# Kernel tuning notes

Measured on AMD Instinct MI355X. Metric: run time of the kernel, lower is better.

The kernel has to match this reference:

```python
import jax, jax.numpy as jnp
import numpy as np

B, S, D = 8, 1024, 1024   # batch, routed-over rows, feature dim (input_dim)
E = 1024                  # output_dim (== S so gather indices are in range)
K = 2                     # top-k
ALPHA = 0.01


def setup_inputs() -> dict:
    key = jax.random.key(0)
    kx, kw = jax.random.split(key)
    x = jax.random.normal(kx, (B, S, D), dtype=jnp.float32)
    # nn.Linear(input_dim, output_dim, bias=False) weight: [E, D]
    W = jax.random.normal(kw, (E, D), dtype=jnp.float32) / np.sqrt(D).astype(np.float32)
    return {"x": x, "W": W}


def reference(x, W):
    # logits = proj(x): [B, S, E]  (temperature == 1.0 -> no scaling)
    logits = jnp.einsum('bsd,ed->bse', x, W)
    probs = jax.nn.softmax(logits, axis=-1)
    topk_probs, topk_idx = jax.lax.top_k(probs, K)            # [B, S, K]
    # router_selections: gather rows of x along dim 1 -> [B, S, K, D]
    sel = x[jnp.arange(B)[:, None, None], topk_idx]
    # y = sum_k topk_probs * selected rows -> [B, S, D]
    y = jnp.einsum('bsk,bskd->bsd', topk_probs, sel)
    # auxiliary load-balance loss
    router_probs = probs.mean(axis=(0, 1))                    # [E]
    counts = jnp.bincount(topk_idx.reshape(-1), length=E).astype(probs.dtype)
    router_fraction = counts / counts.sum()
    aux_loss = ALPHA * E * jnp.sum(router_probs * router_fraction)
    return y, aux_loss
```

## Files before the change

### kernel.cpp

```cpp
#include <hip/hip_runtime.h>

#define MTOK 8192
#define ED   1024

typedef short s16x8 __attribute__((ext_vector_type(8)));
typedef float f32x4 __attribute__((ext_vector_type(4)));
typedef int   i32x4 __attribute__((ext_vector_type(4)));
typedef unsigned short u16x4 __attribute__((ext_vector_type(4)));

__device__ __forceinline__ unsigned short f2bf(float f) {
    unsigned u = __builtin_bit_cast(unsigned, f);
    u += 0x7fff + ((u >> 16) & 1);
    return (unsigned short)(u >> 16);
}
__device__ __forceinline__ float bf2f(unsigned short h) {
    unsigned u = ((unsigned)h) << 16;
    return __builtin_bit_cast(float, u);
}

__global__ __launch_bounds__(256) void split_bf16_kernel(
        const float* __restrict__ src, unsigned short* __restrict__ hi,
        unsigned short* __restrict__ lo, int n4) {
    int idx = blockIdx.x * 256 + threadIdx.x;
    const int stride = gridDim.x * 256;
    for (; idx < n4; idx += stride) {
        float4 v = ((const float4*)src)[idx];
        u16x4 h, l;
        h[0] = f2bf(v.x); l[0] = f2bf(v.x - bf2f(h[0]));
        h[1] = f2bf(v.y); l[1] = f2bf(v.y - bf2f(h[1]));
        h[2] = f2bf(v.z); l[2] = f2bf(v.z - bf2f(h[2]));
        h[3] = f2bf(v.w); l[3] = f2bf(v.w - bf2f(h[3]));
        ((u16x4*)hi)[idx] = h;
        ((u16x4*)lo)[idx] = l;
    }
}

__device__ __forceinline__ void gload16(const void* g, void* l) {
    __builtin_amdgcn_global_load_lds(
        (const __attribute__((address_space(1))) void*)g,
        (__attribute__((address_space(3))) void*)l, 16, 0, 0);
}

__device__ __forceinline__ int cvtpk(float a, float b) {
    int r;
    asm("v_cvt_pk_bf16_f32 %0, %1, %2" : "=v"(r) : "v"(a), "v"(b));
    return r;
}

__global__ __launch_bounds__(256, 2) void gemm_mfma_split_kernel(
        const float* __restrict__ Xf,
        const unsigned short* __restrict__ Whi, const unsigned short* __restrict__ Wlo,
        float* __restrict__ C) {
    __shared__ __align__(16) unsigned char smem[2 * 32768];

    const int bid = blockIdx.x;
    const int xcd = bid & 7;
    const int j   = bid >> 3;
    const int bm  = xcd * 8 + (j >> 3);
    const int bn  = j & 7;

    const int tid  = threadIdx.x;
    const int lane = tid & 63;
    const int wid  = tid >> 6;

    const float* gsrcF = Xf + (size_t)(bm * 128 + wid * 64 + (lane & 15)) * ED
                            + (lane >> 4) * 8;
    const int srow = lane >> 2;
    const int sg   = (lane & 3) ^ ((srow >> 1) & 3);
    const unsigned short* gsrcS =
        ((wid == 3) ? Wlo : Whi) + (size_t)(bn * 128 + srow) * ED + sg * 8;
    unsigned char* const dstU = smem + ((wid < 2) ? wid * 8192
                                                  : 16384 + (wid - 2) * 8192);

#define STAGE(buf, kk)                                                          \
    if (wid < 2) {                                                              \
        _Pragma("unroll")                                                       \
        for (int c = 0; c < 8; ++c)                                             \
            gload16(gsrcF + (kk) + (c >> 1) * (16 * ED) + (c & 1) * 4,          \
                    dstU + (buf) * 32768 + c * 1024);                           \
    } else {                                                                    \
        _Pragma("unroll")                                                       \
        for (int c = 0; c < 8; ++c)                                             \
            gload16(gsrcS + (kk) + c * (16 * ED),                               \
                    dstU + (buf) * 32768 + c * 1024);                           \
    }

    const int wm = wid >> 1, wn = wid & 1;
    const int fr = lane & 15, fg = lane >> 4;
    const int pg = fg ^ ((fr >> 1) & 3);
    const int boff  = ((wn * 64 + fr) * 32 + pg * 8) * 2;
    const int aoffb = wm * 8192 + lane * 16;

    f32x4 acc[4][4] = {};

    STAGE(0, 0);
    asm volatile("s_waitcnt vmcnt(0)" ::: "memory");
    __builtin_amdgcn_s_barrier();

    for (int t = 0; t < 32; ++t) {
        const int cur = t & 1;
        if (t < 31) STAGE(cur ^ 1, (t + 1) * 32);

        const unsigned char* bufb = smem + cur * 32768;

        s16x8 ah[4], al[4], bh[4], bl[4];
#pragma unroll
        for (int i = 0; i < 4; ++i) {
            const float4 f0 = *(const float4*)(bufb + aoffb + i * 2048);
            const float4 f1 = *(const float4*)(bufb + aoffb + i * 2048 + 1024);
            i32x4 h, l;
            h[0] = cvtpk(f0.x, f0.y);
            h[1] = cvtpk(f0.z, f0.w);
            h[2] = cvtpk(f1.x, f1.y);
            h[3] = cvtpk(f1.z, f1.w);
            l[0] = cvtpk(f0.x - __builtin_bit_cast(float, h[0] << 16),
                         f0.y - __builtin_bit_cast(float, h[0] & 0xffff0000));
            l[1] = cvtpk(f0.z - __builtin_bit_cast(float, h[1] << 16),
                         f0.w - __builtin_bit_cast(float, h[1] & 0xffff0000));
            l[2] = cvtpk(f1.x - __builtin_bit_cast(float, h[2] << 16),
                         f1.y - __builtin_bit_cast(float, h[2] & 0xffff0000));
            l[3] = cvtpk(f1.z - __builtin_bit_cast(float, h[3] << 16),
                         f1.w - __builtin_bit_cast(float, h[3] & 0xffff0000));
            ah[i] = __builtin_bit_cast(s16x8, h);
            al[i] = __builtin_bit_cast(s16x8, l);
            bh[i] = *(const s16x8*)(bufb + 16384 + boff + i * 1024);
            bl[i] = *(const s16x8*)(bufb + 24576 + boff + i * 1024);
        }
#pragma unroll
        for (int i = 0; i < 4; ++i)
#pragma unroll
            for (int jj = 0; jj < 4; ++jj) {
                acc[i][jj] = __builtin_amdgcn_mfma_f32_16x16x32_bf16(ah[i], bh[jj], acc[i][jj], 0, 0, 0);
                acc[i][jj] = __builtin_amdgcn_mfma_f32_16x16x32_bf16(ah[i], bl[jj], acc[i][jj], 0, 0, 0);
                acc[i][jj] = __builtin_amdgcn_mfma_f32_16x16x32_bf16(al[i], bh[jj], acc[i][jj], 0, 0, 0);
            }

        asm volatile("s_waitcnt vmcnt(0) lgkmcnt(0)" ::: "memory");
        __builtin_amdgcn_s_barrier();
    }
#undef STAGE

    const int crow = bm * 128 + wm * 64 + fg * 4;
    const int ccol = bn * 128 + wn * 64 + fr;
#pragma unroll
    for (int i = 0; i < 4; ++i)
#pragma unroll
        for (int jj = 0; jj < 4; ++jj)
#pragma unroll
            for (int r = 0; r < 4; ++r)
                C[(size_t)(crow + i * 16 + r) * ED + ccol + jj * 16] = acc[i][jj][r];
}

#define BM 128
#define BN 128
#define BK 32
#define LDA (BM + 4)
#define LDB (BN + 4)

__global__ __launch_bounds__(256) void gemm_logits_kernel(const float* __restrict__ X,
                                                          const float* __restrict__ W,
                                                          float* __restrict__ C) {
    __shared__ float As[BK][LDA];
    __shared__ float Bs[BK][LDB];
    const int bm  = blockIdx.y * BM;
    const int bn  = blockIdx.x * BN;
    const int tid = threadIdx.x;
    const int tx  = tid & 15;
    const int ty  = tid >> 4;
    const int lr  = tid >> 3;
    const int lc  = (tid & 7) << 2;

    float acc[8][8];
#pragma unroll
    for (int i = 0; i < 8; ++i)
#pragma unroll
        for (int j = 0; j < 8; ++j) acc[i][j] = 0.f;

    for (int k0 = 0; k0 < ED; k0 += BK) {
#pragma unroll
        for (int i = 0; i < 4; ++i) {
            const int r = lr + i * 32;
            float4 va = *(const float4*)&X[(size_t)(bm + r) * ED + k0 + lc];
            As[lc + 0][r] = va.x; As[lc + 1][r] = va.y;
            As[lc + 2][r] = va.z; As[lc + 3][r] = va.w;
            float4 vb = *(const float4*)&W[(size_t)(bn + r) * ED + k0 + lc];
            Bs[lc + 0][r] = vb.x; Bs[lc + 1][r] = vb.y;
            Bs[lc + 2][r] = vb.z; Bs[lc + 3][r] = vb.w;
        }
        __syncthreads();
#pragma unroll
        for (int kk = 0; kk < BK; ++kk) {
            float a[8], b[8];
            *(float4*)&a[0] = *(const float4*)&As[kk][ty * 8];
            *(float4*)&a[4] = *(const float4*)&As[kk][ty * 8 + 4];
            *(float4*)&b[0] = *(const float4*)&Bs[kk][tx * 8];
            *(float4*)&b[4] = *(const float4*)&Bs[kk][tx * 8 + 4];
#pragma unroll
            for (int i = 0; i < 8; ++i)
#pragma unroll
                for (int j = 0; j < 8; ++j)
                    acc[i][j] = fmaf(a[i], b[j], acc[i][j]);
        }
        __syncthreads();
    }
#pragma unroll
    for (int i = 0; i < 8; ++i) {
        const int r = bm + ty * 8 + i;
        float4* dst = (float4*)&C[(size_t)r * ED + bn + tx * 8];
        dst[0] = make_float4(acc[i][0], acc[i][1], acc[i][2], acc[i][3]);
        dst[1] = make_float4(acc[i][4], acc[i][5], acc[i][6], acc[i][7]);
    }
}

__device__ __forceinline__ bool better(float v, int i, float bv, int bi) {
    return (v > bv) || (v == bv && i < bi);
}

__global__ __launch_bounds__(256, 8) void softmax_wave_kernel(
        const float* __restrict__ X, float* __restrict__ OUT,
        float* __restrict__ partial, int* __restrict__ counts) {
    __shared__ float L[4 * 1024];
    const int tid  = threadIdx.x;
    const int lane = tid & 63;
    const int w    = tid >> 6;
    const int t    = blockIdx.x * 4 + w;

    const float4* row4 = (const float4*)&OUT[(size_t)t * ED];
    float4 p[4];
#pragma unroll
    for (int i = 0; i < 4; ++i) p[i] = row4[lane + 64 * i];

    float v1 = -1e30f, v2 = -1e30f; int i1 = 0x7fffffff, i2 = 0x7fffffff;
#pragma unroll
    for (int i = 0; i < 4; ++i) {
        const float vv[4] = {p[i].x, p[i].y, p[i].z, p[i].w};
#pragma unroll
        for (int c = 0; c < 4; ++c) {
            const int e = 256 * i + 4 * lane + c;
            const float v = vv[c];
            if (better(v, e, v1, i1)) { v2 = v1; i2 = i1; v1 = v; i1 = e; }
            else if (better(v, e, v2, i2)) { v2 = v; i2 = e; }
        }
    }
#pragma unroll
    for (int off = 32; off; off >>= 1) {
        const float ov1 = __shfl_xor(v1, off); const int oi1 = __shfl_xor(i1, off);
        const float ov2 = __shfl_xor(v2, off); const int oi2 = __shfl_xor(i2, off);
        if (better(ov1, oi1, v1, i1)) {
            float nv2; int ni2;
            if (better(v1, i1, ov2, oi2)) { nv2 = v1; ni2 = i1; }
            else { nv2 = ov2; ni2 = oi2; }
            v1 = ov1; i1 = oi1; v2 = nv2; i2 = ni2;
        } else if (better(ov1, oi1, v2, i2)) { v2 = ov1; i2 = oi1; }
    }
    const float m = v1;

    float s = 0.f;
#pragma unroll
    for (int i = 0; i < 4; ++i) {
        p[i].x = __expf(p[i].x - m); p[i].y = __expf(p[i].y - m);
        p[i].z = __expf(p[i].z - m); p[i].w = __expf(p[i].w - m);
        s += p[i].x + p[i].y + p[i].z + p[i].w;
    }
#pragma unroll
    for (int off = 32; off; off >>= 1) s += __shfl_xor(s, off);
    const float inv = 1.f / s;

#pragma unroll
    for (int i = 0; i < 4; ++i) {
        float4 q = make_float4(p[i].x * inv, p[i].y * inv, p[i].z * inv, p[i].w * inv);
        *(float4*)&L[w * 1024 + i * 256 + lane * 4] = q;
    }

    const float p1 = inv;
    const float p2 = __expf(v2 - m) * inv;
    const int b = t >> 10;
    const float4* x1 = (const float4*)&X[((size_t)(b << 10) + i1) * ED];
    const float4* x2 = (const float4*)&X[((size_t)(b << 10) + i2) * ED];
    float4* yrow = (float4*)&OUT[(size_t)t * ED];
#pragma unroll
    for (int i = 0; i < 4; ++i) {
        const int idx = lane + 64 * i;
        const float4 a = x1[idx];
        const float4 c = x2[idx];
        float4 r;
        r.x = fmaf(p1, a.x, p2 * c.x);
        r.y = fmaf(p1, a.y, p2 * c.y);
        r.z = fmaf(p1, a.z, p2 * c.z);
        r.w = fmaf(p1, a.w, p2 * c.w);
        yrow[idx] = r;
    }

    if (lane == 0) { atomicAdd(&counts[i1], 1); atomicAdd(&counts[i2], 1); }

    __syncthreads();
    float4 s0 = *(float4*)&L[0 * 1024 + tid * 4];
    float4 s1 = *(float4*)&L[1 * 1024 + tid * 4];
    float4 s2 = *(float4*)&L[2 * 1024 + tid * 4];
    float4 s3 = *(float4*)&L[3 * 1024 + tid * 4];
    float4 r;
    r.x = (s0.x + s1.x) + (s2.x + s3.x);
    r.y = (s0.y + s1.y) + (s2.y + s3.y);
    r.z = (s0.z + s1.z) + (s2.z + s3.z);
    r.w = (s0.w + s1.w) + (s2.w + s3.w);
    *(float4*)&partial[(size_t)blockIdx.x * 1024 + tid * 4] = r;
}

__global__ __launch_bounds__(256) void aux1_kernel(const float* __restrict__ partial,
                                                   const int* __restrict__ counts,
                                                   float* __restrict__ dotPartial) {
    __shared__ float red[16][16];
    const int tid = threadIdx.x;
    const int el  = tid & 15;
    const int ch  = tid >> 4;
    const int e   = blockIdx.x * 16 + el;
    float s = 0.f;
    for (int k = 0; k < 128; ++k)
        s += partial[(size_t)(ch * 128 + k) * 1024 + e];
    red[ch][el] = s;
    __syncthreads();
    if (tid < 16) {
        float rs = 0.f;
#pragma unroll
        for (int c = 0; c < 16; ++c) rs += red[c][tid];
        float val = rs * (float)counts[blockIdx.x * 16 + tid];
#pragma unroll
        for (int off = 8; off; off >>= 1) val += __shfl_xor(val, off);
        if (tid == 0) dotPartial[blockIdx.x] = val;
    }
}

__global__ void aux2_kernel(const float* __restrict__ dotPartial, float* __restrict__ out) {
    const int lane = threadIdx.x;
    float v = dotPartial[lane];
#pragma unroll
    for (int off = 32; off; off >>= 1) v += __shfl_xor(v, off);
    if (lane == 0)
        out[(size_t)MTOK * ED] = v * (0.01f * 1024.f / (8192.f * 16384.f));
}

#define TOKS_PER_BLK 16
__global__ __launch_bounds__(256) void softmax_topk_y_kernel(
        const float* __restrict__ X, float* __restrict__ OUT,
        float* __restrict__ router_sum, int* __restrict__ counts) {
    __shared__ float routerLocal[ED];
    __shared__ float redMax[4];
    __shared__ float redSum[4];
    __shared__ float wV1[4]; __shared__ int wI1[4];
    __shared__ float wV2[4]; __shared__ int wI2[4];

    const int tid  = threadIdx.x;
    const int lane = tid & 63;
    const int wave = tid >> 6;

    for (int e = tid; e < ED; e += 256) routerLocal[e] = 0.f;
    __syncthreads();

    const int t0 = blockIdx.x * TOKS_PER_BLK;
    for (int t = t0; t < t0 + TOKS_PER_BLK; ++t) {
        const float* lrow = &OUT[(size_t)t * ED];
        float l[4];
#pragma unroll
        for (int i = 0; i < 4; ++i) l[i] = lrow[tid + i * 256];

        float m = fmaxf(fmaxf(l[0], l[1]), fmaxf(l[2], l[3]));
#pragma unroll
        for (int off = 32; off; off >>= 1) m = fmaxf(m, __shfl_xor(m, off));
        if (lane == 0) redMax[wave] = m;
        __syncthreads();
        m = fmaxf(fmaxf(redMax[0], redMax[1]), fmaxf(redMax[2], redMax[3]));

        float p[4]; float s = 0.f;
#pragma unroll
        for (int i = 0; i < 4; ++i) { p[i] = expf(l[i] - m); s += p[i]; }
#pragma unroll
        for (int off = 32; off; off >>= 1) s += __shfl_xor(s, off);
        if (lane == 0) redSum[wave] = s;

        float v1 = -1e30f, v2 = -1e30f; int i1 = 0x7fffffff, i2 = 0x7fffffff;
#pragma unroll
        for (int i = 0; i < 4; ++i) {
            const float v = l[i]; const int ix = tid + i * 256;
            if (better(v, ix, v1, i1)) { v2 = v1; i2 = i1; v1 = v; i1 = ix; }
            else if (better(v, ix, v2, i2)) { v2 = v; i2 = ix; }
        }
#pragma unroll
        for (int off = 32; off; off >>= 1) {
            const float ov1 = __shfl_xor(v1, off); const int oi1 = __shfl_xor(i1, off);
            const float ov2 = __shfl_xor(v2, off); const int oi2 = __shfl_xor(i2, off);
            if (better(ov1, oi1, v1, i1)) {
                float nv2; int ni2;
                if (better(v1, i1, ov2, oi2)) { nv2 = v1; ni2 = i1; }
                else { nv2 = ov2; ni2 = oi2; }
                v1 = ov1; i1 = oi1; v2 = nv2; i2 = ni2;
            } else if (better(ov1, oi1, v2, i2)) { v2 = ov1; i2 = oi1; }
        }
        if (lane == 0) { wV1[wave] = v1; wI1[wave] = i1; wV2[wave] = v2; wI2[wave] = i2; }
        __syncthreads();

        v1 = wV1[0]; i1 = wI1[0]; v2 = wV2[0]; i2 = wI2[0];
#pragma unroll
        for (int w = 1; w < 4; ++w) {
            const float ov1 = wV1[w]; const int oi1 = wI1[w];
            const float ov2 = wV2[w]; const int oi2 = wI2[w];
            if (better(ov1, oi1, v1, i1)) {
                float nv2; int ni2;
                if (better(v1, i1, ov2, oi2)) { nv2 = v1; ni2 = i1; }
                else { nv2 = ov2; ni2 = oi2; }
                v1 = ov1; i1 = oi1; v2 = nv2; i2 = ni2;
            } else if (better(ov1, oi1, v2, i2)) { v2 = ov1; i2 = oi1; }
        }
        const float stot = redSum[0] + redSum[1] + redSum[2] + redSum[3];
        const float inv = 1.f / stot;

#pragma unroll
        for (int i = 0; i < 4; ++i) routerLocal[tid + i * 256] += p[i] * inv;

        const float p1 = expf(v1 - m) * inv;
        const float p2 = expf(v2 - m) * inv;

        const int b = t >> 10;
        const float4* x1 = (const float4*)&X[((size_t)(b << 10) + i1) * ED];
        const float4* x2 = (const float4*)&X[((size_t)(b << 10) + i2) * ED];
        float4* yrow = (float4*)&OUT[(size_t)t * ED];
        const float4 a = x1[tid];
        const float4 c = x2[tid];
        float4 r;
        r.x = fmaf(p1, a.x, p2 * c.x);
        r.y = fmaf(p1, a.y, p2 * c.y);
        r.z = fmaf(p1, a.z, p2 * c.z);
        r.w = fmaf(p1, a.w, p2 * c.w);
        yrow[tid] = r;

        if (tid == 0) { atomicAdd(&counts[i1], 1); atomicAdd(&counts[i2], 1); }
        __syncthreads();
    }

    for (int e = tid; e < ED; e += 256) atomicAdd(&router_sum[e], routerLocal[e]);
}

__global__ __launch_bounds__(256) void aux_kernel(const float* __restrict__ router_sum,
                                                  const int* __restrict__ counts,
                                                  float* __restrict__ out) {
    __shared__ float red[4];
    const int tid = threadIdx.x;
    float s = 0.f;
    for (int e = tid; e < ED; e += 256)
        s += (router_sum[e] * (1.f / 8192.f)) * ((float)counts[e] * (1.f / 16384.f));
#pragma unroll
    for (int off = 32; off; off >>= 1) s += __shfl_xor(s, off);
    if ((tid & 63) == 0) red[tid >> 6] = s;
    __syncthreads();
    if (tid == 0) out[(size_t)MTOK * ED] = 0.01f * 1024.f * (red[0] + red[1] + red[2] + red[3]);
}

extern "C" void kernel_launch(void* const* d_in, const int* in_sizes, int n_in,
                              void* d_out, int out_size, void* d_ws, size_t ws_size,
                              hipStream_t stream) {
    const float* X = (const float*)d_in[0];
    const float* W = (const float*)d_in[1];
    float* out = (float*)d_out;

    const size_t WS_NEED = (size_t)ED * ED * 2 * sizeof(unsigned short)
                         + (size_t)2048 * 1024 * sizeof(float)
                         + 64 * sizeof(float) + ED * sizeof(int);

    if (ws_size >= WS_NEED) {
        unsigned short* Whi = (unsigned short*)d_ws;
        unsigned short* Wlo = Whi + (size_t)ED * ED;
        float* partial      = (float*)(Wlo + (size_t)ED * ED);
        float* dotPartial   = partial + (size_t)2048 * 1024;
        int*   counts       = (int*)(dotPartial + 64);

        hipMemsetAsync(counts, 0, ED * sizeof(int), stream);
        split_bf16_kernel<<<512, 256, 0, stream>>>(W, Whi, Wlo, ED * ED / 4);
        gemm_mfma_split_kernel<<<512, 256, 0, stream>>>(X, Whi, Wlo, out);
        softmax_wave_kernel<<<MTOK / 4, 256, 0, stream>>>(X, out, partial, counts);
        aux1_kernel<<<64, 256, 0, stream>>>(partial, counts, dotPartial);
        aux2_kernel<<<1, 64, 0, stream>>>(dotPartial, out);
    } else {
        float* router_sum = (float*)d_ws;
        int*   counts     = (int*)((char*)d_ws + ED * sizeof(float));
        hipMemsetAsync(d_ws, 0, ED * (sizeof(float) + sizeof(int)), stream);
        dim3 ggrid(ED / BN, MTOK / BM);
        gemm_logits_kernel<<<ggrid, 256, 0, stream>>>(X, W, out);
        softmax_topk_y_kernel<<<MTOK / TOKS_PER_BLK, 256, 0, stream>>>(X, out, router_sum, counts);
        aux_kernel<<<1, 256, 0, stream>>>(router_sum, counts, out);
    }
}
```

Before: 99.16 us.

## Convert X tile to bf16 hi/lo once per block before staging into LDS

The A (X) operand was previously copied to LDS as fp32 and each wave converted it to bf16 hi/lo pairs at read time. The two waves sharing the same rows therefore repeated the split. Now A is loaded into registers, split once by the loading wave, and written to LDS as swizzled bf16 hi/lo after the MFMAs, so the global load overlaps compute. This removes redundant conversion work and halves LDS read bytes for A. The cost is extra registers for the prefetched floats and LDS writes issued from VGPRs instead of direct global-to-LDS loads.

```diff
diff --git a/kernel.cpp b/kernel.cpp
--- a/kernel.cpp
+++ b/kernel.cpp
@@ -47,6 +47,23 @@
     return r;
 }
 
+__device__ __forceinline__ void cvt_write(void* dstHi, void* dstLo,
+                                          const float4 f0, const float4 f1) {
+    i32x4 h, l;
+    h[0] = cvtpk(f0.x, f0.y); h[1] = cvtpk(f0.z, f0.w);
+    h[2] = cvtpk(f1.x, f1.y); h[3] = cvtpk(f1.z, f1.w);
+    l[0] = cvtpk(f0.x - __builtin_bit_cast(float, h[0] << 16),
+                 f0.y - __builtin_bit_cast(float, h[0] & 0xffff0000));
+    l[1] = cvtpk(f0.z - __builtin_bit_cast(float, h[1] << 16),
+                 f0.w - __builtin_bit_cast(float, h[1] & 0xffff0000));
+    l[2] = cvtpk(f1.x - __builtin_bit_cast(float, h[2] << 16),
+                 f1.y - __builtin_bit_cast(float, h[2] & 0xffff0000));
+    l[3] = cvtpk(f1.z - __builtin_bit_cast(float, h[3] << 16),
+                 f1.w - __builtin_bit_cast(float, h[3] & 0xffff0000));
+    *(i32x4*)dstHi = h;
+    *(i32x4*)dstLo = l;
+}
+
 __global__ __launch_bounds__(256, 2) void gemm_mfma_split_kernel(
         const float* __restrict__ Xf,
         const unsigned short* __restrict__ Whi, const unsigned short* __restrict__ Wlo,
@@ -63,68 +80,64 @@
     const int lane = tid & 63;
     const int wid  = tid >> 6;
 
-    const float* gsrcF = Xf + (size_t)(bm * 128 + wid * 64 + (lane & 15)) * ED
-                            + (lane >> 4) * 8;
     const int srow = lane >> 2;
-    const int sg   = (lane & 3) ^ ((srow >> 1) & 3);
-    const unsigned short* gsrcS =
-        ((wid == 3) ? Wlo : Whi) + (size_t)(bn * 128 + srow) * ED + sg * 8;
-    unsigned char* const dstU = smem + ((wid < 2) ? wid * 8192
-                                                  : 16384 + (wid - 2) * 8192);
-
-#define STAGE(buf, kk)                                                          \
-    if (wid < 2) {                                                              \
-        _Pragma("unroll")                                                       \
-        for (int c = 0; c < 8; ++c)                                             \
-            gload16(gsrcF + (kk) + (c >> 1) * (16 * ED) + (c & 1) * 4,          \
-                    dstU + (buf) * 32768 + c * 1024);                           \
-    } else {                                                                    \
-        _Pragma("unroll")                                                       \
-        for (int c = 0; c < 8; ++c)                                             \
-            gload16(gsrcS + (kk) + c * (16 * ED),                               \
-                    dstU + (buf) * 32768 + c * 1024);                           \
-    }
+    const int sg   = (lane & 3) ^ ((lane >> 3) & 3);
+    const float* gA = Xf + (size_t)(bm * 128 + wid * 32 + srow) * ED + sg * 8;
+    const unsigned short* gB = ((wid < 2) ? Whi : Wlo)
+            + (size_t)(bn * 128 + (wid & 1) * 64 + srow) * ED + sg * 8;
+    unsigned char* const dB = smem + 16384 + ((wid < 2) ? 0 : 8192) + (wid & 1) * 4096;
+
+    float4 fA0, fA1, fA2, fA3;
+
+#define ALOAD(kk)                                                    \
+    fA0 = *(const float4*)(gA + (kk));                               \
+    fA1 = *(const float4*)(gA + (kk) + 4);                           \
+    fA2 = *(const float4*)(gA + (kk) + 16 * 1024);                   \
+    fA3 = *(const float4*)(gA + (kk) + 16 * 1024 + 4);
+
+#define BSTAGE(buf, kk)                                              \
+    _Pragma("unroll")                                                \
+    for (int c = 0; c < 4; ++c)                                      \
+        gload16(gB + (kk) + c * (16 * ED), dB + (buf) * 32768 + c * 1024);
+
+#define AWRITE(buf)                                                              \
+    cvt_write(smem + (buf) * 32768 + (2 * wid) * 1024 + lane * 16,               \
+              smem + (buf) * 32768 + 8192 + (2 * wid) * 1024 + lane * 16,        \
+              fA0, fA1);                                                         \
+    cvt_write(smem + (buf) * 32768 + (2 * wid + 1) * 1024 + lane * 16,           \
+              smem + (buf) * 32768 + 8192 + (2 * wid + 1) * 1024 + lane * 16,    \
+              fA2, fA3);
 
     const int wm = wid >> 1, wn = wid & 1;
     const int fr = lane & 15, fg = lane >> 4;
     const int pg = fg ^ ((fr >> 1) & 3);
-    const int boff  = ((wn * 64 + fr) * 32 + pg * 8) * 2;
-    const int aoffb = wm * 8192 + lane * 16;
+    const int aoff = (wm * 64 + fr) * 32 + pg * 8;
+    const int boff = (wn * 64 + fr) * 32 + pg * 8;
 
     f32x4 acc[4][4] = {};
 
-    STAGE(0, 0);
-    asm volatile("s_waitcnt vmcnt(0)" ::: "memory");
+    ALOAD(0);
+    BSTAGE(0, 0);
+    AWRITE(0);
+    asm volatile("s_waitcnt vmcnt(0) lgkmcnt(0)" ::: "memory");
     __builtin_amdgcn_s_barrier();
 
     for (int t = 0; t < 32; ++t) {
         const int cur = t & 1;
-        if (t < 31) STAGE(cur ^ 1, (t + 1) * 32);
-
-        const unsigned char* bufb = smem + cur * 32768;
+        if (t < 31) { ALOAD((t + 1) * 32); BSTAGE(cur ^ 1, (t + 1) * 32); }
+
+        const unsigned short* Ah = (const unsigned short*)(smem + cur * 32768);
+        const unsigned short* Al = Ah + 4096;
+        const unsigned short* Bh = Ah + 8192;
+        const unsigned short* Bl = Ah + 12288;
 
         s16x8 ah[4], al[4], bh[4], bl[4];
 #pragma unroll
         for (int i = 0; i < 4; ++i) {
-            const float4 f0 = *(const float4*)(bufb + aoffb + i * 2048);
-            const float4 f1 = *(const float4*)(bufb + aoffb + i * 2048 + 1024);
-            i32x4 h, l;
-            h[0] = cvtpk(f0.x, f0.y);
-            h[1] = cvtpk(f0.z, f0.w);
-            h[2] = cvtpk(f1.x, f1.y);
-            h[3] = cvtpk(f1.z, f1.w);
-            l[0] = cvtpk(f0.x - __builtin_bit_cast(float, h[0] << 16),
-                         f0.y - __builtin_bit_cast(float, h[0] & 0xffff0000));
-            l[1] = cvtpk(f0.z - __builtin_bit_cast(float, h[1] << 16),
-                         f0.w - __builtin_bit_cast(float, h[1] & 0xffff0000));
-            l[2] = cvtpk(f1.x - __builtin_bit_cast(float, h[2] << 16),
-                         f1.y - __builtin_bit_cast(float, h[2] & 0xffff0000));
-            l[3] = cvtpk(f1.z - __builtin_bit_cast(float, h[3] << 16),
-                         f1.w - __builtin_bit_cast(float, h[3] & 0xffff0000));
-            ah[i] = __builtin_bit_cast(s16x8, h);
-            al[i] = __builtin_bit_cast(s16x8, l);
-            bh[i] = *(const s16x8*)(bufb + 16384 + boff + i * 1024);
-            bl[i] = *(const s16x8*)(bufb + 24576 + boff + i * 1024);
+            ah[i] = *(const s16x8*)&Ah[aoff + i * 512];
+            al[i] = *(const s16x8*)&Al[aoff + i * 512];
+            bh[i] = *(const s16x8*)&Bh[boff + i * 512];
+            bl[i] = *(const s16x8*)&Bl[boff + i * 512];
         }
 #pragma unroll
         for (int i = 0; i < 4; ++i)
@@ -135,10 +148,14 @@
                 acc[i][jj] = __builtin_amdgcn_mfma_f32_16x16x32_bf16(al[i], bh[jj], acc[i][jj], 0, 0, 0);
             }
 
+        if (t < 31) AWRITE(cur ^ 1);
+
         asm volatile("s_waitcnt vmcnt(0) lgkmcnt(0)" ::: "memory");
         __builtin_amdgcn_s_barrier();
     }
-#undef STAGE
+#undef ALOAD
+#undef BSTAGE
+#undef AWRITE
 
     const int crow = bm * 128 + wm * 64 + fg * 4;
     const int ccol = bn * 128 + wn * 64 + fr;
```

Measured after the change: 93.70 us. -5.5%, faster.
